# Performance work log

Measured on AMD Instinct MI355X. Metric: run time of the kernel, lower is better.

Reference implementation:

```python
import jax, jax.numpy as jnp
import numpy as np

N_NODES = 10000
N_EDGES = 320000
D = 128      # node/edge feature dim
H = 512      # MLP hidden width


def _mlp(x, W1, b1, W2, b2):
    return jax.nn.relu(x @ W1 + b1) @ W2 + b2


def setup_inputs() -> dict:
    key = jax.random.key(0)
    ks = jax.random.split(key, 8)
    s = lambda fan_in: 1.0 / np.sqrt(fan_in)
    return {
        "x": jax.random.normal(ks[0], (N_NODES, D), jnp.float32),
        "edge_index": jax.random.randint(ks[1], (2, N_EDGES), 0, N_NODES, jnp.int64),
        "edge_attr": jax.random.normal(ks[2], (N_EDGES, D), jnp.float32),
        "We1": jax.random.normal(ks[3], (3 * D, H), jnp.float32) * s(3 * D),
        "be1": jnp.zeros((H,), jnp.float32),
        "We2": jax.random.normal(ks[4], (H, D), jnp.float32) * s(H),
        "be2": jnp.zeros((D,), jnp.float32),
        "Wn1": jax.random.normal(ks[5], (2 * D, H), jnp.float32) * s(2 * D),
        "bn1": jnp.zeros((H,), jnp.float32),
        "Wn2": jax.random.normal(ks[6], (H, D), jnp.float32) * s(H),
        "bn2": jnp.zeros((D,), jnp.float32),
    }


def reference(x, edge_index, edge_attr, We1, be1, We2, be2, Wn1, bn1, Wn2, bn2):
    senders = edge_index[0]
    receivers = edge_index[1]
    # gather -> edge MLP
    edge_inputs = jnp.concatenate([x[senders], x[receivers], edge_attr], axis=-1)  # [E, 3D]
    updated_edge_attr = _mlp(edge_inputs, We1, be1, We2, be2)                      # [E, D]
    # scatter-add into receiving nodes
    aggregated = jax.ops.segment_sum(updated_edge_attr, receivers, num_segments=x.shape[0])  # [N, D]
    # node MLP
    node_inputs = jnp.concatenate([x, aggregated], axis=-1)                        # [N, 2D]
    updated_nodes = _mlp(node_inputs, Wn1, bn1, Wn2, bn2)                          # [N, D]
    return updated_nodes, updated_edge_attr
```

## Files before the change

### kernel.cpp

```cpp
#include <hip/hip_runtime.h>
#include <hip/hip_bf16.h>

#define N_NODES 10000
#define N_EDGES 320000
#define D 128
#define H 512

typedef __bf16 bf16x8 __attribute__((ext_vector_type(8)));
typedef float f32x4 __attribute__((ext_vector_type(4)));
typedef unsigned short u16x8 __attribute__((ext_vector_type(8)));

__device__ __forceinline__ unsigned short f2bf(float f) {
    union { float f; unsigned u; } v; v.f = f;
    unsigned r = v.u + 0x7fffu + ((v.u >> 16) & 1u);
    return (unsigned short)(r >> 16);
}

__global__ void cast_x_kernel(const float* __restrict__ x, unsigned short* __restrict__ xb) {
    int t = blockIdx.x * 256 + threadIdx.x;
    float4 v = reinterpret_cast<const float4*>(x)[t];
    ushort4 o;
    o.x = f2bf(v.x); o.y = f2bf(v.y); o.z = f2bf(v.z); o.w = f2bf(v.w);
    reinterpret_cast<ushort4*>(xb)[t] = o;
}

__global__ void swizzle_w_kernel(const float* __restrict__ W, unsigned short* __restrict__ out,
                                 int K, int Nn) {
    int t = blockIdx.x * 256 + threadIdx.x;
    int total = (K >> 5) * (Nn >> 4) * 64;
    if (t >= total) return;
    int lane = t & 63;
    int tile = t >> 6;
    int ntiles = Nn >> 4;
    int nt = tile % ntiles;
    int kt = tile / ntiles;
    int k0 = kt * 32 + (lane >> 4) * 8;
    int n  = nt * 16 + (lane & 15);
    unsigned short tmp[8];
#pragma unroll
    for (int j = 0; j < 8; ++j) tmp[j] = f2bf(W[(size_t)(k0 + j) * Nn + n]);
    ushort4* dst = reinterpret_cast<ushort4*>(out + (size_t)t * 8);
    dst[0] = *reinterpret_cast<ushort4*>(&tmp[0]);
    dst[1] = *reinterpret_cast<ushort4*>(&tmp[4]);
}

__global__ __launch_bounds__(256) void edge_mlp_kernel(
    const unsigned short* __restrict__ xb,
    const int* __restrict__ eidx,
    const float* __restrict__ edge_attr,
    const unsigned short* __restrict__ We1s,
    const float* __restrict__ be1,
    const unsigned short* __restrict__ We2s,
    const float* __restrict__ be2,
    float* __restrict__ out_edges,
    float* __restrict__ agg)
{
    __shared__ unsigned short sA[64 * 392];
    __shared__ unsigned short sH[64 * 136];

    const int tid = threadIdx.x;
    const int wave = tid >> 6, lane = tid & 63;
    const int e0 = blockIdx.x * 64;
    const int l15 = lane & 15;
    const int q8 = (lane >> 4) * 8;

#pragma unroll
    for (int seg = 0; seg < 2; ++seg) {
        for (int c = tid; c < 1024; c += 256) {
            int row = c >> 4;
            int off = (c & 15) << 3;
            int e = e0 + row;
            int node = eidx[seg * N_EDGES + e];
            *reinterpret_cast<bf16x8*>(&sA[row * 392 + seg * 128 + off]) =
                *reinterpret_cast<const bf16x8*>(&xb[(size_t)node * 128 + off]);
        }
    }
    for (int c = tid; c < 1024; c += 256) {
        int row = c >> 4;
        int off = (c & 15) << 3;
        int e = e0 + row;
        const float4* src = reinterpret_cast<const float4*>(&edge_attr[(size_t)e * 128 + off]);
        float4 v0 = src[0], v1 = src[1];
        u16x8 o;
        o[0] = f2bf(v0.x); o[1] = f2bf(v0.y); o[2] = f2bf(v0.z); o[3] = f2bf(v0.w);
        o[4] = f2bf(v1.x); o[5] = f2bf(v1.y); o[6] = f2bf(v1.z); o[7] = f2bf(v1.w);
        *reinterpret_cast<u16x8*>(&sA[row * 392 + 256 + off]) = o;
    }
    __syncthreads();

    f32x4 acc2[2][4];
#pragma unroll
    for (int nn = 0; nn < 2; ++nn)
#pragma unroll
        for (int mt = 0; mt < 4; ++mt) acc2[nn][mt] = (f32x4){0.f, 0.f, 0.f, 0.f};

#pragma unroll 1
    for (int h = 0; h < 4; ++h) {
        f32x4 acc1[2][4];
#pragma unroll
        for (int nn = 0; nn < 2; ++nn)
#pragma unroll
            for (int mt = 0; mt < 4; ++mt) acc1[nn][mt] = (f32x4){0.f, 0.f, 0.f, 0.f};

#pragma unroll
        for (int kt = 0; kt < 12; ++kt) {
            bf16x8 a[4];
#pragma unroll
            for (int mt = 0; mt < 4; ++mt)
                a[mt] = *reinterpret_cast<const bf16x8*>(&sA[(mt * 16 + l15) * 392 + kt * 32 + q8]);
#pragma unroll
            for (int nn = 0; nn < 2; ++nn) {
                int ntile = h * 8 + wave * 2 + nn;
                bf16x8 b = *reinterpret_cast<const bf16x8*>(
                    &We1s[(((size_t)kt * 32 + ntile) * 64 + lane) * 8]);
#pragma unroll
                for (int mt = 0; mt < 4; ++mt)
                    acc1[nn][mt] = __builtin_amdgcn_mfma_f32_16x16x32_bf16(a[mt], b, acc1[nn][mt], 0, 0, 0);
            }
        }

        __syncthreads();
#pragma unroll
        for (int nn = 0; nn < 2; ++nn) {
            int cc = (wave * 2 + nn) * 16 + l15;
            float bias = be1[h * 128 + cc];
#pragma unroll
            for (int mt = 0; mt < 4; ++mt)
#pragma unroll
                for (int r = 0; r < 4; ++r) {
                    float v = acc1[nn][mt][r] + bias;
                    v = v > 0.f ? v : 0.f;
                    int row = mt * 16 + (lane >> 4) * 4 + r;
                    sH[row * 136 + cc] = f2bf(v);
                }
        }
        __syncthreads();

#pragma unroll
        for (int kt = 0; kt < 4; ++kt) {
            bf16x8 a[4];
#pragma unroll
            for (int mt = 0; mt < 4; ++mt)
                a[mt] = *reinterpret_cast<const bf16x8*>(&sH[(mt * 16 + l15) * 136 + kt * 32 + q8]);
#pragma unroll
            for (int nn = 0; nn < 2; ++nn) {
                int ntile = wave * 2 + nn;
                bf16x8 b = *reinterpret_cast<const bf16x8*>(
                    &We2s[(((size_t)(h * 4 + kt) * 8 + ntile) * 64 + lane) * 8]);
#pragma unroll
                for (int mt = 0; mt < 4; ++mt)
                    acc2[nn][mt] = __builtin_amdgcn_mfma_f32_16x16x32_bf16(a[mt], b, acc2[nn][mt], 0, 0, 0);
            }
        }
    }

#pragma unroll
    for (int nn = 0; nn < 2; ++nn) {
        int cc = (wave * 2 + nn) * 16 + l15;
        float bias = be2[cc];
#pragma unroll
        for (int mt = 0; mt < 4; ++mt)
#pragma unroll
            for (int r = 0; r < 4; ++r) {
                int row = mt * 16 + (lane >> 4) * 4 + r;
                int e = e0 + row;
                float v = acc2[nn][mt][r] + bias;
                out_edges[(size_t)e * 128 + cc] = v;
                int recv = eidx[N_EDGES + e];
                atomicAdd(&agg[(size_t)recv * 128 + cc], v);
            }
    }
}

__global__ __launch_bounds__(256) void node_mlp_kernel(
    const unsigned short* __restrict__ xb,
    const float* __restrict__ agg,
    const unsigned short* __restrict__ Wn1s,
    const float* __restrict__ bn1,
    const unsigned short* __restrict__ Wn2s,
    const float* __restrict__ bn2,
    float* __restrict__ out_nodes)
{
    __shared__ unsigned short sA[64 * 264];
    __shared__ unsigned short sH[64 * 136];

    const int tid = threadIdx.x;
    const int wave = tid >> 6, lane = tid & 63;
    const int n0 = blockIdx.x * 64;
    const int l15 = lane & 15;
    const int q8 = (lane >> 4) * 8;

    for (int c = tid; c < 1024; c += 256) {
        int row = c >> 4;
        int off = (c & 15) << 3;
        int node = n0 + row;
        bf16x8 v = {};
        if (node < N_NODES)
            v = *reinterpret_cast<const bf16x8*>(&xb[(size_t)node * 128 + off]);
        *reinterpret_cast<bf16x8*>(&sA[row * 264 + off]) = v;
    }
    for (int c = tid; c < 1024; c += 256) {
        int row = c >> 4;
        int off = (c & 15) << 3;
        int node = n0 + row;
        u16x8 o = {0, 0, 0, 0, 0, 0, 0, 0};
        if (node < N_NODES) {
            const float4* src = reinterpret_cast<const float4*>(&agg[(size_t)node * 128 + off]);
            float4 v0 = src[0], v1 = src[1];
            o[0] = f2bf(v0.x); o[1] = f2bf(v0.y); o[2] = f2bf(v0.z); o[3] = f2bf(v0.w);
            o[4] = f2bf(v1.x); o[5] = f2bf(v1.y); o[6] = f2bf(v1.z); o[7] = f2bf(v1.w);
        }
        *reinterpret_cast<u16x8*>(&sA[row * 264 + 128 + off]) = o;
    }
    __syncthreads();

    f32x4 acc2[2][4];
#pragma unroll
    for (int nn = 0; nn < 2; ++nn)
#pragma unroll
        for (int mt = 0; mt < 4; ++mt) acc2[nn][mt] = (f32x4){0.f, 0.f, 0.f, 0.f};

#pragma unroll 1
    for (int h = 0; h < 4; ++h) {
        f32x4 acc1[2][4];
#pragma unroll
        for (int nn = 0; nn < 2; ++nn)
#pragma unroll
            for (int mt = 0; mt < 4; ++mt) acc1[nn][mt] = (f32x4){0.f, 0.f, 0.f, 0.f};

#pragma unroll
        for (int kt = 0; kt < 8; ++kt) {
            bf16x8 a[4];
#pragma unroll
            for (int mt = 0; mt < 4; ++mt)
                a[mt] = *reinterpret_cast<const bf16x8*>(&sA[(mt * 16 + l15) * 264 + kt * 32 + q8]);
#pragma unroll
            for (int nn = 0; nn < 2; ++nn) {
                int ntile = h * 8 + wave * 2 + nn;
                bf16x8 b = *reinterpret_cast<const bf16x8*>(
                    &Wn1s[(((size_t)kt * 32 + ntile) * 64 + lane) * 8]);
#pragma unroll
                for (int mt = 0; mt < 4; ++mt)
                    acc1[nn][mt] = __builtin_amdgcn_mfma_f32_16x16x32_bf16(a[mt], b, acc1[nn][mt], 0, 0, 0);
            }
        }

        __syncthreads();
#pragma unroll
        for (int nn = 0; nn < 2; ++nn) {
            int cc = (wave * 2 + nn) * 16 + l15;
            float bias = bn1[h * 128 + cc];
#pragma unroll
            for (int mt = 0; mt < 4; ++mt)
#pragma unroll
                for (int r = 0; r < 4; ++r) {
                    float v = acc1[nn][mt][r] + bias;
                    v = v > 0.f ? v : 0.f;
                    int row = mt * 16 + (lane >> 4) * 4 + r;
                    sH[row * 136 + cc] = f2bf(v);
                }
        }
        __syncthreads();

#pragma unroll
        for (int kt = 0; kt < 4; ++kt) {
            bf16x8 a[4];
#pragma unroll
            for (int mt = 0; mt < 4; ++mt)
                a[mt] = *reinterpret_cast<const bf16x8*>(&sH[(mt * 16 + l15) * 136 + kt * 32 + q8]);
#pragma unroll
            for (int nn = 0; nn < 2; ++nn) {
                int ntile = wave * 2 + nn;
                bf16x8 b = *reinterpret_cast<const bf16x8*>(
                    &Wn2s[(((size_t)(h * 4 + kt) * 8 + ntile) * 64 + lane) * 8]);
#pragma unroll
                for (int mt = 0; mt < 4; ++mt)
                    acc2[nn][mt] = __builtin_amdgcn_mfma_f32_16x16x32_bf16(a[mt], b, acc2[nn][mt], 0, 0, 0);
            }
        }
    }

#pragma unroll
    for (int nn = 0; nn < 2; ++nn) {
        int cc = (wave * 2 + nn) * 16 + l15;
        float bias = bn2[cc];
#pragma unroll
        for (int mt = 0; mt < 4; ++mt)
#pragma unroll
            for (int r = 0; r < 4; ++r) {
                int row = mt * 16 + (lane >> 4) * 4 + r;
                int node = n0 + row;
                if (node < N_NODES)
                    out_nodes[(size_t)node * 128 + cc] = acc2[nn][mt][r] + bias;
            }
    }
}

extern "C" void kernel_launch(void* const* d_in, const int* in_sizes, int n_in,
                              void* d_out, int out_size, void* d_ws, size_t ws_size,
                              hipStream_t stream) {
    const float* x         = (const float*)d_in[0];
    const int*   eidx      = (const int*)d_in[1];
    const float* edge_attr = (const float*)d_in[2];
    const float* We1       = (const float*)d_in[3];
    const float* be1       = (const float*)d_in[4];
    const float* We2       = (const float*)d_in[5];
    const float* be2       = (const float*)d_in[6];
    const float* Wn1       = (const float*)d_in[7];
    const float* bn1       = (const float*)d_in[8];
    const float* Wn2       = (const float*)d_in[9];
    const float* bn2       = (const float*)d_in[10];
    float* out = (float*)d_out;

    char* ws = (char*)d_ws;
    size_t off = 0;
    auto alloc = [&](size_t bytes) {
        void* p = ws + off;
        off += (bytes + 255) & ~(size_t)255;
        return p;
    };
    unsigned short* xb   = (unsigned short*)alloc((size_t)N_NODES * D * 2);
    unsigned short* We1s = (unsigned short*)alloc((size_t)384 * 512 * 2);
    unsigned short* We2s = (unsigned short*)alloc((size_t)512 * 128 * 2);
    unsigned short* Wn1s = (unsigned short*)alloc((size_t)256 * 512 * 2);
    unsigned short* Wn2s = (unsigned short*)alloc((size_t)512 * 128 * 2);
    float*          agg  = (float*)alloc((size_t)N_NODES * D * 4);

    hipMemsetAsync(agg, 0, (size_t)N_NODES * D * sizeof(float), stream);
    cast_x_kernel<<<(N_NODES * D / 4 + 255) / 256, 256, 0, stream>>>(x, xb);
    swizzle_w_kernel<<<(12 * 32 * 64 + 255) / 256, 256, 0, stream>>>(We1, We1s, 384, 512);
    swizzle_w_kernel<<<(16 * 8 * 64 + 255) / 256, 256, 0, stream>>>(We2, We2s, 512, 128);
    swizzle_w_kernel<<<(8 * 32 * 64 + 255) / 256, 256, 0, stream>>>(Wn1, Wn1s, 256, 512);
    swizzle_w_kernel<<<(16 * 8 * 64 + 255) / 256, 256, 0, stream>>>(Wn2, Wn2s, 512, 128);

    edge_mlp_kernel<<<N_EDGES / 64, 256, 0, stream>>>(
        xb, eidx, edge_attr, We1s, be1, We2s, be2, out + (size_t)N_NODES * D, agg);
    node_mlp_kernel<<<(N_NODES + 63) / 64, 256, 0, stream>>>(
        xb, agg, Wn1s, bn1, Wn2s, bn2, out);
}
```

Baseline: 723.5 us.

## Compute full hidden layer per block and merge prep kernels into one launch

The edge and node MLP kernels now compute all 512 hidden columns in one pass, with each wave holding 8x4 accumulator tiles, so the A-tile fragments are read from LDS once instead of four times. The whole hidden layer is staged in a single shared buffer, written as packed bf16 pairs via a lane shuffle, and then fed to the second GEMM. The five setup launches (cast, memset, four swizzles) are merged into one kernel. The larger per-wave accumulator set raises register pressure. The launch_bounds(256,2) hint may force spills or limit occupancy, and the bigger LDS footprint reduces how many blocks fit per CU.

Result: slower. 759.6 us (+5.0%).

```diff
diff --git a/kernel.cpp b/kernel.cpp
--- a/kernel.cpp
+++ b/kernel.cpp
@@ -16,19 +16,8 @@
     return (unsigned short)(r >> 16);
 }
 
-__global__ void cast_x_kernel(const float* __restrict__ x, unsigned short* __restrict__ xb) {
-    int t = blockIdx.x * 256 + threadIdx.x;
-    float4 v = reinterpret_cast<const float4*>(x)[t];
-    ushort4 o;
-    o.x = f2bf(v.x); o.y = f2bf(v.y); o.z = f2bf(v.z); o.w = f2bf(v.w);
-    reinterpret_cast<ushort4*>(xb)[t] = o;
-}
-
-__global__ void swizzle_w_kernel(const float* __restrict__ W, unsigned short* __restrict__ out,
-                                 int K, int Nn) {
-    int t = blockIdx.x * 256 + threadIdx.x;
-    int total = (K >> 5) * (Nn >> 4) * 64;
-    if (t >= total) return;
+__device__ __forceinline__ void swz(const float* __restrict__ W, unsigned short* __restrict__ out,
+                                    int K, int Nn, int t) {
     int lane = t & 63;
     int tile = t >> 6;
     int ntiles = Nn >> 4;
@@ -44,7 +33,36 @@
     dst[1] = *reinterpret_cast<ushort4*>(&tmp[4]);
 }
 
-__global__ __launch_bounds__(256) void edge_mlp_kernel(
+__global__ __launch_bounds__(256) void precompute_kernel(
+    const float* __restrict__ x, unsigned short* __restrict__ xb,
+    const float* __restrict__ We1, unsigned short* __restrict__ We1s,
+    const float* __restrict__ We2, unsigned short* __restrict__ We2s,
+    const float* __restrict__ Wn1, unsigned short* __restrict__ Wn1s,
+    const float* __restrict__ Wn2, unsigned short* __restrict__ Wn2s,
+    float* __restrict__ agg)
+{
+    int b = blockIdx.x, tid = threadIdx.x;
+    if (b < 1250) {
+        int t = b * 256 + tid;
+        float4 v = reinterpret_cast<const float4*>(x)[t];
+        ushort4 o;
+        o.x = f2bf(v.x); o.y = f2bf(v.y); o.z = f2bf(v.z); o.w = f2bf(v.w);
+        reinterpret_cast<ushort4*>(xb)[t] = o;
+    } else if (b < 2500) {
+        int t = (b - 1250) * 256 + tid;
+        reinterpret_cast<float4*>(agg)[t] = (float4){0.f, 0.f, 0.f, 0.f};
+    } else if (b < 2596) {
+        swz(We1, We1s, 384, 512, (b - 2500) * 256 + tid);
+    } else if (b < 2628) {
+        swz(We2, We2s, 512, 128, (b - 2596) * 256 + tid);
+    } else if (b < 2692) {
+        swz(Wn1, Wn1s, 256, 512, (b - 2628) * 256 + tid);
+    } else {
+        swz(Wn2, Wn2s, 512, 128, (b - 2692) * 256 + tid);
+    }
+}
+
+__global__ __launch_bounds__(256, 2) void edge_mlp_kernel(
     const unsigned short* __restrict__ xb,
     const int* __restrict__ eidx,
     const float* __restrict__ edge_attr,
@@ -55,36 +73,85 @@
     float* __restrict__ out_edges,
     float* __restrict__ agg)
 {
-    __shared__ unsigned short sA[64 * 392];
-    __shared__ unsigned short sH[64 * 136];
+    __shared__ unsigned short smem[64 * 520];
 
     const int tid = threadIdx.x;
     const int wave = tid >> 6, lane = tid & 63;
+    const int l15 = lane & 15, quad = lane >> 4;
+    const int q8 = quad * 8;
     const int e0 = blockIdx.x * 64;
-    const int l15 = lane & 15;
-    const int q8 = (lane >> 4) * 8;
 
 #pragma unroll
     for (int seg = 0; seg < 2; ++seg) {
         for (int c = tid; c < 1024; c += 256) {
             int row = c >> 4;
             int off = (c & 15) << 3;
-            int e = e0 + row;
-            int node = eidx[seg * N_EDGES + e];
-            *reinterpret_cast<bf16x8*>(&sA[row * 392 + seg * 128 + off]) =
+            int node = eidx[seg * N_EDGES + e0 + row];
+            *reinterpret_cast<bf16x8*>(&smem[row * 392 + seg * 128 + off]) =
                 *reinterpret_cast<const bf16x8*>(&xb[(size_t)node * 128 + off]);
         }
     }
     for (int c = tid; c < 1024; c += 256) {
         int row = c >> 4;
         int off = (c & 15) << 3;
-        int e = e0 + row;
-        const float4* src = reinterpret_cast<const float4*>(&edge_attr[(size_t)e * 128 + off]);
+        const float4* src = reinterpret_cast<const float4*>(&edge_attr[((size_t)(e0 + row)) * 128 + off]);
         float4 v0 = src[0], v1 = src[1];
         u16x8 o;
         o[0] = f2bf(v0.x); o[1] = f2bf(v0.y); o[2] = f2bf(v0.z); o[3] = f2bf(v0.w);
         o[4] = f2bf(v1.x); o[5] = f2bf(v1.y); o[6] = f2bf(v1.z); o[7] = f2bf(v1.w);
-        *reinterpret_cast<u16x8*>(&sA[row * 392 + 256 + off]) = o;
+        *reinterpret_cast<u16x8*>(&smem[row * 392 + 256 + off]) = o;
+    }
+    __syncthreads();
+
+    f32x4 acc1[8][4];
+#pragma unroll
+    for (int nn = 0; nn < 8; ++nn)
+#pragma unroll
+        for (int mt = 0; mt < 4; ++mt) acc1[nn][mt] = (f32x4){0.f, 0.f, 0.f, 0.f};
+
+#pragma unroll 2
+    for (int kt = 0; kt < 12; ++kt) {
+        bf16x8 a[4];
+#pragma unroll
+        for (int mt = 0; mt < 4; ++mt)
+            a[mt] = *reinterpret_cast<const bf16x8*>(&smem[(mt * 16 + l15) * 392 + kt * 32 + q8]);
+#pragma unroll
+        for (int nn = 0; nn < 8; ++nn) {
+            bf16x8 b = *reinterpret_cast<const bf16x8*>(
+                &We1s[(((size_t)kt * 32 + wave * 8 + nn) * 64 + lane) * 8]);
+#pragma unroll
+            for (int mt = 0; mt < 4; ++mt)
+                acc1[nn][mt] = __builtin_amdgcn_mfma_f32_16x16x32_bf16(a[mt], b, acc1[nn][mt], 0, 0, 0);
+        }
+    }
+    __syncthreads();
+
+    const int rs = (lane & 1) * 2;
+#pragma unroll
+    for (int nn = 0; nn < 8; ++nn) {
+        int cc = wave * 128 + nn * 16 + l15;
+        float bias = be1[cc];
+        int cp = cc & ~1;
+#pragma unroll
+        for (int mt = 0; mt < 4; ++mt) {
+            float v[4], p[4];
+#pragma unroll
+            for (int r = 0; r < 4; ++r) {
+                float t = acc1[nn][mt][r] + bias;
+                v[r] = t > 0.f ? t : 0.f;
+            }
+#pragma unroll
+            for (int r = 0; r < 4; ++r) p[r] = __shfl_xor(v[r], 1, 64);
+#pragma unroll
+            for (int r2 = 0; r2 < 2; ++r2) {
+                int r = rs + r2;
+                float lo = (lane & 1) ? p[r] : v[r];
+                float hi = (lane & 1) ? v[r] : p[r];
+                unsigned d = (unsigned)f2bf(lo) | ((unsigned)f2bf(hi) << 16);
+                int row = mt * 16 + quad * 4 + r;
+                *reinterpret_cast<unsigned*>(&smem[row * 520 + cp]) = d;
+            }
+        }
     }
     __syncthreads();
 
@@ -94,85 +161,42 @@
 #pragma unroll
         for (int mt = 0; mt < 4; ++mt) acc2[nn][mt] = (f32x4){0.f, 0.f, 0.f, 0.f};
 
-#pragma unroll 1
-    for (int h = 0; h < 4; ++h) {
-        f32x4 acc1[2][4];
-#pragma unroll
-        for (int nn = 0; nn < 2; ++nn)
-#pragma unroll
-            for (int mt = 0; mt < 4; ++mt) acc1[nn][mt] = (f32x4){0.f, 0.f, 0.f, 0.f};
-
-#pragma unroll
-        for (int kt = 0; kt < 12; ++kt) {
-            bf16x8 a[4];
+#pragma unroll 2
+    for (int kt = 0; kt < 16; ++kt) {
+        bf16x8 a[4];
+#pragma unroll
+        for (int mt = 0; mt < 4; ++mt)
+            a[mt] = *reinterpret_cast<const bf16x8*>(&smem[(mt * 16 + l15) * 520 + kt * 32 + q8]);
+#pragma unroll
+        for (int nn = 0; nn < 2; ++nn) {
+            bf16x8 b = *reinterpret_cast<const bf16x8*>(
+                &We2s[(((size_t)kt * 8 + wave * 2 + nn) * 64 + lane) * 8]);
 #pragma unroll
             for (int mt = 0; mt < 4; ++mt)
-                a[mt] = *reinterpret_cast<const bf16x8*>(&sA[(mt * 16 + l15) * 392 + kt * 32 + q8]);
+                acc2[nn][mt] = __builtin_amdgcn_mfma_f32_16x16x32_bf16(a[mt], b, acc2[nn][mt], 0, 0, 0);
+        }
+    }
+
+    float bias2[2] = { be2[wave * 32 + l15], be2[wave * 32 + 16 + l15] };
+#pragma unroll
+    for (int mt = 0; mt < 4; ++mt) {
+#pragma unroll
+        for (int r = 0; r < 4; ++r) {
+            int row = mt * 16 + quad * 4 + r;
+            int e = e0 + row;
+            int recv = eidx[N_EDGES + e];
 #pragma unroll
             for (int nn = 0; nn < 2; ++nn) {
-                int ntile = h * 8 + wave * 2 + nn;
-                bf16x8 b = *reinterpret_cast<const bf16x8*>(
-                    &We1s[(((size_t)kt * 32 + ntile) * 64 + lane) * 8]);
-#pragma unroll
-                for (int mt = 0; mt < 4; ++mt)
-                    acc1[nn][mt] = __builtin_amdgcn_mfma_f32_16x16x32_bf16(a[mt], b, acc1[nn][mt], 0, 0, 0);
-            }
-        }
-
-        __syncthreads();
-#pragma unroll
-        for (int nn = 0; nn < 2; ++nn) {
-            int cc = (wave * 2 + nn) * 16 + l15;
-            float bias = be1[h * 128 + cc];
-#pragma unroll
-            for (int mt = 0; mt < 4; ++mt)
-#pragma unroll
-                for (int r = 0; r < 4; ++r) {
-                    float v = acc1[nn][mt][r] + bias;
-                    v = v > 0.f ? v : 0.f;
-                    int row = mt * 16 + (lane >> 4) * 4 + r;
-                    sH[row * 136 + cc] = f2bf(v);
-                }
-        }
-        __syncthreads();
-
-#pragma unroll
-        for (int kt = 0; kt < 4; ++kt) {
-            bf16x8 a[4];
-#pragma unroll
-            for (int mt = 0; mt < 4; ++mt)
-                a[mt] = *reinterpret_cast<const bf16x8*>(&sH[(mt * 16 + l15) * 136 + kt * 32 + q8]);
-#pragma unroll
-            for (int nn = 0; nn < 2; ++nn) {
-                int ntile = wave * 2 + nn;
-                bf16x8 b = *reinterpret_cast<const bf16x8*>(
-                    &We2s[(((size_t)(h * 4 + kt) * 8 + ntile) * 64 + lane) * 8]);
-#pragma unroll
-                for (int mt = 0; mt < 4; ++mt)
-                    acc2[nn][mt] = __builtin_amdgcn_mfma_f32_16x16x32_bf16(a[mt], b, acc2[nn][mt], 0, 0, 0);
-            }
-        }
-    }
-
-#pragma unroll
-    for (int nn = 0; nn < 2; ++nn) {
-        int cc = (wave * 2 + nn) * 16 + l15;
-        float bias = be2[cc];
-#pragma unroll
-        for (int mt = 0; mt < 4; ++mt)
-#pragma unroll
-            for (int r = 0; r < 4; ++r) {
-                int row = mt * 16 + (lane >> 4) * 4 + r;
-                int e = e0 + row;
-                float v = acc2[nn][mt][r] + bias;
+                int cc = wave * 32 + nn * 16 + l15;
+                float v = acc2[nn][mt][r] + bias2[nn];
                 out_edges[(size_t)e * 128 + cc] = v;
-                int recv = eidx[N_EDGES + e];
                 atomicAdd(&agg[(size_t)recv * 128 + cc], v);
             }
-    }
-}
-
-__global__ __launch_bounds__(256) void node_mlp_kernel(
+        }
+    }
+}
+
+__global__ __launch_bounds__(256, 2) void node_mlp_kernel(
     const unsigned short* __restrict__ xb,
     const float* __restrict__ agg,
     const unsigned short* __restrict__ Wn1s,
@@ -181,14 +205,13 @@
     const float* __restrict__ bn2,
     float* __restrict__ out_nodes)
 {
-    __shared__ unsigned short sA[64 * 264];
-    __shared__ unsigned short sH[64 * 136];
+    __shared__ unsigned short smem[64 * 520];
 
     const int tid = threadIdx.x;
     const int wave = tid >> 6, lane = tid & 63;
+    const int l15 = lane & 15, quad = lane >> 4;
+    const int q8 = quad * 8;
     const int n0 = blockIdx.x * 64;
-    const int l15 = lane & 15;
-    const int q8 = (lane >> 4) * 8;
 
     for (int c = tid; c < 1024; c += 256) {
         int row = c >> 4;
@@ -197,7 +220,7 @@
         bf16x8 v = {};
         if (node < N_NODES)
             v = *reinterpret_cast<const bf16x8*>(&xb[(size_t)node * 128 + off]);
-        *reinterpret_cast<bf16x8*>(&sA[row * 264 + off]) = v;
+        *reinterpret_cast<bf16x8*>(&smem[row * 264 + off]) = v;
     }
     for (int c = tid; c < 1024; c += 256) {
         int row = c >> 4;
@@ -210,7 +233,59 @@
             o[0] = f2bf(v0.x); o[1] = f2bf(v0.y); o[2] = f2bf(v0.z); o[3] = f2bf(v0.w);
             o[4] = f2bf(v1.x); o[5] = f2bf(v1.y); o[6] = f2bf(v1.z); o[7] = f2bf(v1.w);
         }
-        *reinterpret_cast<u16x8*>(&sA[row * 264 + 128 + off]) = o;
+        *reinterpret_cast<u16x8*>(&smem[row * 264 + 128 + off]) = o;
+    }
+    __syncthreads();
+
+    f32x4 acc1[8][4];
+#pragma unroll
+    for (int nn = 0; nn < 8; ++nn)
+#pragma unroll
+        for (int mt = 0; mt < 4; ++mt) acc1[nn][mt] = (f32x4){0.f, 0.f, 0.f, 0.f};
+
+#pragma unroll 2
+    for (int kt = 0; kt < 8; ++kt) {
+        bf16x8 a[4];
+#pragma unroll
+        for (int mt = 0; mt < 4; ++mt)
+            a[mt] = *reinterpret_cast<const bf16x8*>(&smem[(mt * 16 + l15) * 264 + kt * 32 + q8]);
+#pragma unroll
+        for (int nn = 0; nn < 8; ++nn) {
+            bf16x8 b = *reinterpret_cast<const bf16x8*>(
+                &Wn1s[(((size_t)kt * 32 + wave * 8 + nn) * 64 + lane) * 8]);
+#pragma unroll
+            for (int mt = 0; mt < 4; ++mt)
+                acc1[nn][mt] = __builtin_amdgcn_mfma_f32_16x16x32_bf16(a[mt], b, acc1[nn][mt], 0, 0, 0);
+        }
+    }
+    __syncthreads();
+
+    const int rs = (lane & 1) * 2;
+#pragma unroll
+    for (int nn = 0; nn < 8; ++nn) {
+        int cc = wave * 128 + nn * 16 + l15;
+        float bias = bn1[cc];
+        int cp = cc & ~1;
+#pragma unroll
+        for (int mt = 0; mt < 4; ++mt) {
+            float v[4], p[4];
+#pragma unroll
+            for (int r = 0; r < 4; ++r) {
+                float t = acc1[nn][mt][r] + bias;
+                v[r] = t > 0.f ? t : 0.f;
+            }
+#pragma unroll
+            for (int r = 0; r < 4; ++r) p[r] = __shfl_xor(v[r], 1, 64);
+#pragma unroll
+            for (int r2 = 0; r2 < 2; ++r2) {
+                int r = rs + r2;
+                float lo = (lane & 1) ? p[r] : v[r];
+                float hi = (lane & 1) ? v[r] : p[r];
+                unsigned d = (unsigned)f2bf(lo) | ((unsigned)f2bf(hi) << 16);
+                int row = mt * 16 + quad * 4 + r;
+                *reinterpret_cast<unsigned*>(&smem[row * 520 + cp]) = d;
+            }
+        }
     }
     __syncthreads();
 
@@ -220,79 +295,37 @@
 #pragma unroll
         for (int mt = 0; mt < 4; ++mt) acc2[nn][mt] = (f32x4){0.f, 0.f, 0.f, 0.f};
 
-#pragma unroll 1
-    for (int h = 0; h < 4; ++h) {
-        f32x4 acc1[2][4];
-#pragma unroll
-        for (int nn = 0; nn < 2; ++nn)
-#pragma unroll
-            for (int mt = 0; mt < 4; ++mt) acc1[nn][mt] = (f32x4){0.f, 0.f, 0.f, 0.f};
-
-#pragma unroll
-        for (int kt = 0; kt < 8; ++kt) {
-            bf16x8 a[4];
+#pragma unroll 2
+    for (int kt = 0; kt < 16; ++kt) {
+        bf16x8 a[4];
+#pragma unroll
+        for (int mt = 0; mt < 4; ++mt)
+            a[mt] = *reinterpret_cast<const bf16x8*>(&smem[(mt * 16 + l15) * 520 + kt * 32 + q8]);
+#pragma unroll
+        for (int nn = 0; nn < 2; ++nn) {
+            bf16x8 b = *reinterpret_cast<const bf16x8*>(
+                &Wn2s[(((size_t)kt * 8 + wave * 2 + nn) * 64 + lane) * 8]);
 #pragma unroll
             for (int mt = 0; mt < 4; ++mt)
-                a[mt] = *reinterpret_cast<const bf16x8*>(&sA[(mt * 16 + l15) * 264 + kt * 32 + q8]);
-#pragma unroll
-            for (int nn = 0; nn < 2; ++nn) {
-                int ntile = h * 8 + wave * 2 + nn;
-                bf16x8 b = *reinterpret_cast<const bf16x8*>(
-                    &Wn1s[(((size_t)kt * 32 + ntile) * 64 + lane) * 8]);
-#pragma unroll
-                for (int mt = 0; mt < 4; ++mt)
-                    acc1[nn][mt] = __builtin_amdgcn_mfma_f32_16x16x32_bf16(a[mt], b, acc1[nn][mt], 0, 0, 0);
-            }
-        }
-
-        __syncthreads();
-#pragma unroll
-        for (int nn = 0; nn < 2; ++nn) {
-            int cc = (wave * 2 + nn) * 16 + l15;
-            float bias = bn1[h * 128 + cc];
-#pragma unroll
-            for (int mt = 0; mt < 4; ++mt)
-#pragma unroll
-                for (int r = 0; r < 4; ++r) {
-                    float v = acc1[nn][mt][r] + bias;
-                    v = v > 0.f ? v : 0.f;
-                    int row = mt * 16 + (lane >> 4) * 4 + r;
-                    sH[row * 136 + cc] = f2bf(v);
+                acc2[nn][mt] = __builtin_amdgcn_mfma_f32_16x16x32_bf16(a[mt], b, acc2[nn][mt], 0, 0, 0);
+        }
+    }
+
+    float bias2[2] = { bn2[wave * 32 + l15], bn2[wave * 32 + 16 + l15] };
+#pragma unroll
+    for (int mt = 0; mt < 4; ++mt) {
+#pragma unroll
+        for (int r = 0; r < 4; ++r) {
+            int row = mt * 16 + quad * 4 + r;
+            int node = n0 + row;
+            if (node < N_NODES) {
+#pragma unroll
+                for (int nn = 0; nn < 2; ++nn) {
+                    int cc = wave * 32 + nn * 16 + l15;
+                    out_nodes[(size_t)node * 128 + cc] = acc2[nn][mt][r] + bias2[nn];
                 }
-        }
-        __syncthreads();
-
-#pragma unroll
-        for (int kt = 0; kt < 4; ++kt) {
-            bf16x8 a[4];
-#pragma unroll
-            for (int mt = 0; mt < 4; ++mt)
-                a[mt] = *reinterpret_cast<const bf16x8*>(&sH[(mt * 16 + l15) * 136 + kt * 32 + q8]);
-#pragma unroll
-            for (int nn = 0; nn < 2; ++nn) {
-                int ntile = wave * 2 + nn;
-                bf16x8 b = *reinterpret_cast<const bf16x8*>(
-                    &Wn2s[(((size_t)(h * 4 + kt) * 8 + ntile) * 64 + lane) * 8]);
-#pragma unroll
-                for (int mt = 0; mt < 4; ++mt)
-                    acc2[nn][mt] = __builtin_amdgcn_mfma_f32_16x16x32_bf16(a[mt], b, acc2[nn][mt], 0, 0, 0);
-            }
-        }
-    }
-
-#pragma unroll
-    for (int nn = 0; nn < 2; ++nn) {
-        int cc = (wave * 2 + nn) * 16 + l15;
-        float bias = bn2[cc];
-#pragma unroll
-        for (int mt = 0; mt < 4; ++mt)
-#pragma unroll
-            for (int r = 0; r < 4; ++r) {
-                int row = mt * 16 + (lane >> 4) * 4 + r;
-                int node = n0 + row;
-                if (node < N_NODES)
-                    out_nodes[(size_t)node * 128 + cc] = acc2[nn][mt][r] + bias;
-            }
+            }
+        }
     }
 }
 
@@ -326,13 +359,8 @@
     unsigned short* Wn2s = (unsigned short*)alloc((size_t)512 * 128 * 2);
     float*          agg  = (float*)alloc((size_t)N_NODES * D * 4);
 
-    hipMemsetAsync(agg, 0, (size_t)N_NODES * D * sizeof(float), stream);
-    cast_x_kernel<<<(N_NODES * D / 4 + 255) / 256, 256, 0, stream>>>(x, xb);
-    swizzle_w_kernel<<<(12 * 32 * 64 + 255) / 256, 256, 0, stream>>>(We1, We1s, 384, 512);
-    swizzle_w_kernel<<<(16 * 8 * 64 + 255) / 256, 256, 0, stream>>>(We2, We2s, 512, 128);
-    swizzle_w_kernel<<<(8 * 32 * 64 + 255) / 256, 256, 0, stream>>>(Wn1, Wn1s, 256, 512);
-    swizzle_w_kernel<<<(16 * 8 * 64 + 255) / 256, 256, 0, stream>>>(Wn2, Wn2s, 512, 128);
-
+    precompute_kernel<<<2724, 256, 0, stream>>>(x, xb, We1, We1s, We2, We2s,
+                                                Wn1, Wn1s, Wn2, Wn2s, agg);
     edge_mlp_kernel<<<N_EDGES / 64, 256, 0, stream>>>(
         xb, eidx, edge_attr, We1s, be1, We2s, be2, out + (size_t)N_NODES * D, agg);
     node_mlp_kernel<<<(N_NODES + 63) / 64, 256, 0, stream>>>(
```
